# Kernel optimization log

Measured on AMD Instinct MI355X. Metric: run time of the kernel, lower is better.

## Reference

```python
import jax, jax.numpy as jnp
import numpy as np

D = 1536; H = 12; DH = 128; B = 1; S_TXT = 512; S_IMG = 1024; S = S_TXT + S_IMG; FF = 4 * D
EPS = 1e-6


def setup_inputs() -> dict:
    key = jax.random.key(0)
    ks = iter(jax.random.split(key, 64))
    def nrm(shape, s=1.0):
        return jax.random.normal(next(ks), shape, jnp.float32) * s
    w = 0.02
    inp = {}
    inp["hidden_states"] = nrm((B, S_IMG, D))
    inp["encoder_hidden_states"] = nrm((B, S_TXT, D))
    inp["temb"] = nrm((B, D))
    ang = jax.random.uniform(next(ks), (B, S, DH // 2), jnp.float32, 0.0, 2.0 * np.pi)
    c, s = jnp.cos(ang), jnp.sin(ang)
    rot = jnp.stack([jnp.stack([c, -s], -1), jnp.stack([s, c], -1)], -2)  # [B,S,DH/2,2,2]
    inp["image_rotary_emb"] = rot.reshape(1, 1, B * S, DH // 2, 2, 2)
    inp["adaln_img_w"] = nrm((D, 6 * D), w); inp["adaln_img_b"] = jnp.zeros((6 * D,), jnp.float32)
    inp["adaln_txt_w"] = nrm((D, 6 * D), w); inp["adaln_txt_b"] = jnp.zeros((6 * D,), jnp.float32)
    inp["qkv_img_w"] = nrm((D, 3 * D), w); inp["qkv_img_b"] = jnp.zeros((3 * D,), jnp.float32)
    inp["qkv_txt_w"] = nrm((D, 3 * D), w); inp["qkv_txt_b"] = jnp.zeros((3 * D,), jnp.float32)
    inp["q_norm_img"] = jnp.ones((DH,), jnp.float32); inp["k_norm_img"] = jnp.ones((DH,), jnp.float32)
    inp["q_norm_txt"] = jnp.ones((DH,), jnp.float32); inp["k_norm_txt"] = jnp.ones((DH,), jnp.float32)
    inp["out_img_w"] = nrm((D, D), w); inp["out_img_b"] = jnp.zeros((D,), jnp.float32)
    inp["out_txt_w"] = nrm((D, D), w); inp["out_txt_b"] = jnp.zeros((D,), jnp.float32)
    inp["mlp_img_w1"] = nrm((D, FF), w); inp["mlp_img_b1"] = jnp.zeros((FF,), jnp.float32)
    inp["mlp_img_w2"] = nrm((FF, D), w); inp["mlp_img_b2"] = jnp.zeros((D,), jnp.float32)
    inp["mlp_txt_w1"] = nrm((D, FF), w); inp["mlp_txt_b1"] = jnp.zeros((FF,), jnp.float32)
    inp["mlp_txt_w2"] = nrm((FF, D), w); inp["mlp_txt_b2"] = jnp.zeros((D,), jnp.float32)
    return inp


def _ln(x):  # LayerNorm, no affine
    m = jnp.mean(x, -1, keepdims=True)
    v = jnp.mean(jnp.square(x - m), -1, keepdims=True)
    return (x - m) * jax.lax.rsqrt(v + EPS)


def _rms(x, w):  # per-head RMSNorm
    return x * jax.lax.rsqrt(jnp.mean(jnp.square(x), -1, keepdims=True) + EPS) * w


def _rope(x, rot):  # x [B,H,S,DH], rot [B,S,DH/2,2,2]
    xp = x.reshape(*x.shape[:-1], DH // 2, 2)
    out = jnp.einsum('bsdij,bhsdj->bhsdi', rot, xp)
    return out.reshape(x.shape)


def _qkv(x, w, b, qn, kn):  # -> q,k,v each [B,H,S,DH]
    bb, ss, _ = x.shape
    qkv = (x @ w + b).reshape(bb, ss, 3, H, DH).transpose(2, 0, 3, 1, 4)
    q, k, v = qkv[0], qkv[1], qkv[2]
    return _rms(q, qn), _rms(k, kn), v


def _block(hidden_states, encoder_hidden_states, temb, rot,
           adaln_img_w, adaln_img_b, adaln_txt_w, adaln_txt_b,
           qkv_img_w, qkv_img_b, qkv_txt_w, qkv_txt_b,
           q_norm_img, k_norm_img, q_norm_txt, k_norm_txt,
           out_img_w, out_img_b, out_txt_w, out_txt_b,
           mlp_img_w1, mlp_img_b1, mlp_img_w2, mlp_img_b2,
           mlp_txt_w1, mlp_txt_b1, mlp_txt_w2, mlp_txt_b2):
    bsz = hidden_states.shape[0]
    s_txt = encoder_hidden_states.shape[1]
    t = jax.nn.silu(temb)
    emb_i = t @ adaln_img_w + adaln_img_b
    emb_t = t @ adaln_txt_w + adaln_txt_b
    sh_i, sc_i, g_i, shm_i, scm_i, gm_i = [e[:, None, :] for e in jnp.split(emb_i, 6, -1)]
    sh_t, sc_t, g_t, shm_t, scm_t, gm_t = [e[:, None, :] for e in jnp.split(emb_t, 6, -1)]

    n_img = _ln(hidden_states) * (1.0 + sc_i) + sh_i
    n_txt = _ln(encoder_hidden_states) * (1.0 + sc_t) + sh_t

    qi, ki, vi = _qkv(n_img, qkv_img_w, qkv_img_b, q_norm_img, k_norm_img)
    qt, kt, vt = _qkv(n_txt, qkv_txt_w, qkv_txt_b, q_norm_txt, k_norm_txt)
    q = jnp.concatenate([qt, qi], axis=2)
    k = jnp.concatenate([kt, ki], axis=2)
    v = jnp.concatenate([vt, vi], axis=2)

    rot = rot.reshape(bsz, q.shape[2], DH // 2, 2, 2)
    q = _rope(q, rot)
    k = _rope(k, rot)

    scale = 1.0 / np.sqrt(DH)
    attn = jax.nn.softmax(jnp.einsum('bhqd,bhkd->bhqk', q, k) * scale, axis=-1)
    o = jnp.einsum('bhqk,bhkd->bhqd', attn, v)          # [B,H,S,DH]
    o = o.transpose(0, 2, 1, 3).reshape(bsz, -1, D)     # [B,S,D]
    a_txt, a_img = o[:, :s_txt], o[:, s_txt:]

    hidden_states = hidden_states + g_i * (a_img @ out_img_w + out_img_b)
    encoder_hidden_states = encoder_hidden_states + g_t * (a_txt @ out_txt_w + out_txt_b)

    n2_img = _ln(hidden_states) * (1.0 + scm_i) + shm_i
    ff_img = jax.nn.gelu(n2_img @ mlp_img_w1 + mlp_img_b1, approximate=True) @ mlp_img_w2 + mlp_img_b2
    hidden_states = hidden_states + gm_i * ff_img

    n2_txt = _ln(encoder_hidden_states) * (1.0 + scm_t) + shm_t
    ff_txt = jax.nn.gelu(n2_txt @ mlp_txt_w1 + mlp_txt_b1, approximate=True) @ mlp_txt_w2 + mlp_txt_b2
    encoder_hidden_states = encoder_hidden_states + gm_t * ff_txt

    return jnp.concatenate([encoder_hidden_states, hidden_states], axis=1)


def reference(hidden_states, encoder_hidden_states, temb, image_rotary_emb,
              adaln_img_w, adaln_img_b, adaln_txt_w, adaln_txt_b,
              qkv_img_w, qkv_img_b, qkv_txt_w, qkv_txt_b,
              q_norm_img, k_norm_img, q_norm_txt, k_norm_txt,
              out_img_w, out_img_b, out_txt_w, out_txt_b,
              mlp_img_w1, mlp_img_b1, mlp_img_w2, mlp_img_b2,
              mlp_txt_w1, mlp_txt_b1, mlp_txt_w2, mlp_txt_b2):
    s_txt = encoder_hidden_states.shape[1]
    out = _block(hidden_states, encoder_hidden_states, temb, image_rotary_emb,
                 adaln_img_w, adaln_img_b, adaln_txt_w, adaln_txt_b,
                 qkv_img_w, qkv_img_b, qkv_txt_w, qkv_txt_b,
                 q_norm_img, k_norm_img, q_norm_txt, k_norm_txt,
                 out_img_w, out_img_b, out_txt_w, out_txt_b,
                 mlp_img_w1, mlp_img_b1, mlp_img_w2, mlp_img_b2,
                 mlp_txt_w1, mlp_txt_b1, mlp_txt_w2, mlp_txt_b2)
    return (out[:, :s_txt], out[:, s_txt:])
```

## Files before the change

kernel.cpp:

```cpp
#include <hip/hip_runtime.h>
#include <hip/hip_bf16.h>

typedef __bf16 bf16_t;
typedef __attribute__((ext_vector_type(4))) float f32x4;
typedef __attribute__((ext_vector_type(8))) bf16_t bf16x8;
typedef __attribute__((ext_vector_type(4))) bf16_t bf16x4;
typedef __attribute__((ext_vector_type(2))) bf16_t bf16x2;

#define D_MODEL 1536
#define NH 12
#define DHD 128
#define S_TXT 512
#define S_TOT 1536
#define FF_DIM 6144
#define KVSPLIT 4

__device__ inline void gload16(const void* g, void* l) {
    __builtin_amdgcn_global_load_lds((const __attribute__((address_space(1))) unsigned int*)g,
                                     (__attribute__((address_space(3))) unsigned int*)l, 16, 0, 0);
}

__global__ __launch_bounds__(256)
void adaln_p(const float* __restrict__ temb,
             const float* __restrict__ w_img, const float* __restrict__ w_txt,
             float* __restrict__ part) {
    __shared__ float t[192];
    int tid = threadIdx.x;
    int k0 = blockIdx.y * 192;
    if (tid < 192) {
        float x = temb[k0 + tid];
        t[tid] = x / (1.0f + __expf(-x));
    }
    __syncthreads();
    int n_g = blockIdx.x * 256 + tid;
    bool img = n_g < 9216;
    const float* W = img ? w_img : w_txt;
    int n = img ? n_g : n_g - 9216;
    float acc = 0.f;
    for (int kk = 0; kk < 192; kk += 4) {
        acc += t[kk]     * W[(size_t)(k0 + kk) * 9216 + n];
        acc += t[kk + 1] * W[(size_t)(k0 + kk + 1) * 9216 + n];
        acc += t[kk + 2] * W[(size_t)(k0 + kk + 2) * 9216 + n];
        acc += t[kk + 3] * W[(size_t)(k0 + kk + 3) * 9216 + n];
    }
    part[(size_t)blockIdx.y * 18432 + n_g] = acc;
}

__global__ __launch_bounds__(256)
void adaln_r(const float* __restrict__ part,
             const float* __restrict__ b_img, const float* __restrict__ b_txt,
             float* __restrict__ emb_img, float* __restrict__ emb_txt) {
    int n_g = blockIdx.x * 256 + threadIdx.x;
    float a = 0.f;
#pragma unroll
    for (int kc = 0; kc < 8; ++kc) a += part[(size_t)kc * 18432 + n_g];
    if (n_g < 9216) emb_img[n_g] = a + b_img[n_g];
    else            emb_txt[n_g - 9216] = a + b_txt[n_g - 9216];
}

__global__ __launch_bounds__(256)
void ln_mod(const float* __restrict__ src_txt, const float* __restrict__ src_img,
            const float* __restrict__ emb_t, const float* __restrict__ emb_i,
            int sh_c, int sc_c, bf16_t* __restrict__ out) {
    int row = blockIdx.x;
    bool txt = row < S_TXT;
    const float* src = txt ? src_txt + (size_t)row * D_MODEL
                           : src_img + (size_t)(row - S_TXT) * D_MODEL;
    const float* emb = txt ? emb_t : emb_i;
    int tid = threadIdx.x;
    float2 v[3];
    float s = 0.f, sq = 0.f;
#pragma unroll
    for (int i = 0; i < 3; ++i) {
        v[i] = *(const float2*)(src + tid * 2 + 512 * i);
        s  += v[i].x + v[i].y;
        sq += v[i].x * v[i].x + v[i].y * v[i].y;
    }
#pragma unroll
    for (int off = 32; off > 0; off >>= 1) {
        s  += __shfl_down(s, off);
        sq += __shfl_down(sq, off);
    }
    __shared__ float red[8];
    int wave = tid >> 6, lane = tid & 63;
    if (lane == 0) { red[wave] = s; red[4 + wave] = sq; }
    __syncthreads();
    float ts = red[0] + red[1] + red[2] + red[3];
    float tq = red[4] + red[5] + red[6] + red[7];
    float mean = ts * (1.0f / D_MODEL);
    float var  = tq * (1.0f / D_MODEL) - mean * mean;
    float rstd = rsqrtf(var + 1e-6f);
    bf16_t* op = out + (size_t)row * D_MODEL;
#pragma unroll
    for (int i = 0; i < 3; ++i) {
        int c0 = tid * 2 + 512 * i;
        bf16x2 r;
        r[0] = (bf16_t)((v[i].x - mean) * rstd * (1.0f + emb[sc_c * D_MODEL + c0])     + emb[sh_c * D_MODEL + c0]);
        r[1] = (bf16_t)((v[i].y - mean) * rstd * (1.0f + emb[sc_c * D_MODEL + c0 + 1]) + emb[sh_c * D_MODEL + c0 + 1]);
        *(bf16x2*)(op + c0) = r;
    }
}

template <int K, int N>
__global__ __launch_bounds__(256)
void conv_wt(const float* __restrict__ w_t, const float* __restrict__ w_i,
             bf16_t* __restrict__ dst) {
    __shared__ float tile[64][65];
    const float* src = blockIdx.z ? w_i : w_t;
    bf16_t* d = dst + (size_t)blockIdx.z * N * K;
    int bn = blockIdx.x * 64, bk = blockIdx.y * 64;
    int tid = threadIdx.x;
#pragma unroll
    for (int j = 0; j < 4; ++j) {
        int k = (tid >> 4) + 16 * j, c4 = tid & 15;
        float4 v = *(const float4*)(src + (size_t)(bk + k) * N + bn + c4 * 4);
        tile[k][c4 * 4 + 0] = v.x;
        tile[k][c4 * 4 + 1] = v.y;
        tile[k][c4 * 4 + 2] = v.z;
        tile[k][c4 * 4 + 3] = v.w;
    }
    __syncthreads();
#pragma unroll
    for (int j = 0; j < 4; ++j) {
        int n = (tid >> 4) + 16 * j, k4 = tid & 15;
        bf16x4 o;
        o[0] = (bf16_t)tile[k4 * 4 + 0][n];
        o[1] = (bf16_t)tile[k4 * 4 + 1][n];
        o[2] = (bf16_t)tile[k4 * 4 + 2][n];
        o[3] = (bf16_t)tile[k4 * 4 + 3][n];
        *(bf16x4*)(d + (size_t)(bn + n) * K + bk + k4 * 4) = o;
    }
}

template <int EPI>
__global__ __launch_bounds__(512)
void gemmW(const bf16_t* __restrict__ A, int lda,
           const bf16_t* __restrict__ Wt, int ldw, int wimg_off,
           const float* __restrict__ bias_t, const float* __restrict__ bias_i,
           bf16_t* __restrict__ out, bf16_t* __restrict__ out_alt, int ldo, int Ks) {
    __shared__ bf16_t As[128 * 64];
    __shared__ bf16_t Bs[128 * 64];
    const int tid = threadIdx.x;

    const int nbx = gridDim.x;
    const int lb0 = blockIdx.y * nbx + blockIdx.x;
    const int CC = nbx >> 2;
    const int xcd = lb0 & 7, c = lb0 >> 3;
    const int bmT = (xcd & 1) * 6 + (c % 6);
    const int bnT = (xcd >> 1) * CC + (c / 6);
    const int bm = bmT * 128, bn = bnT * 128;
    const int koff = blockIdx.z * Ks;

    const bool txt = bm < S_TXT;
    const bf16_t* W = txt ? Wt : Wt + wimg_off;
    const float* bias = txt ? bias_t : bias_i;
    const int wid = tid >> 6, lane = tid & 63;
    const int wm = wid >> 1, wn = wid & 1;
    const int lr = lane & 15, lg = lane >> 4;

    const int srow = wid * 8 + (lane >> 3);
    const int csrc = ((lane & 7) ^ ((lane >> 3) & 7)) * 8;
    const bf16_t* pA0 = A + (size_t)(bm + srow) * lda + koff + csrc;
    const bf16_t* pA1 = pA0 + (size_t)64 * lda;
    const bf16_t* pB0 = W + (size_t)(bn + srow) * ldw + koff + csrc;
    const bf16_t* pB1 = pB0 + (size_t)64 * ldw;
    const int ldst = (wid * 8) * 64;

    int offA[2][2], offB[4][2];
#pragma unroll
    for (int m = 0; m < 2; ++m)
#pragma unroll
        for (int kk = 0; kk < 2; ++kk)
            offA[m][kk] = (wm * 32 + m * 16 + lr) * 64 + (((kk * 4 + lg) ^ (lr & 7)) * 8);
#pragma unroll
    for (int n = 0; n < 4; ++n)
#pragma unroll
        for (int kk = 0; kk < 2; ++kk)
            offB[n][kk] = (wn * 64 + n * 16 + lr) * 64 + (((kk * 4 + lg) ^ (lr & 7)) * 8);

    f32x4 acc[2][4] = {};
    const int nt = Ks >> 6;

    for (int t = 0; t < nt; ++t) {
        gload16(pA0, &As[ldst]);
        gload16(pA1, &As[ldst + 64 * 64]);
        gload16(pB0, &Bs[ldst]);
        gload16(pB1, &Bs[ldst + 64 * 64]);
        pA0 += 64; pA1 += 64; pB0 += 64; pB1 += 64;
        __syncthreads();
#pragma unroll
        for (int kk = 0; kk < 2; ++kk) {
            bf16x8 af[2], bfm[4];
#pragma unroll
            for (int m = 0; m < 2; ++m) af[m] = *(const bf16x8*)&As[offA[m][kk]];
#pragma unroll
            for (int n = 0; n < 4; ++n) bfm[n] = *(const bf16x8*)&Bs[offB[n][kk]];
#pragma unroll
            for (int m = 0; m < 2; ++m)
#pragma unroll
                for (int n = 0; n < 4; ++n)
                    acc[m][n] = __builtin_amdgcn_mfma_f32_16x16x32_bf16(af[m], bfm[n], acc[m][n], 0, 0, 0);
        }
        __syncthreads();
    }

    bf16_t* obase = out;
    if constexpr (EPI == 3)
        obase = (blockIdx.z < 2) ? out + (size_t)blockIdx.z * S_TOT * ldo
                                 : out_alt + (size_t)(blockIdx.z - 2) * S_TOT * ldo;
#pragma unroll
    for (int m = 0; m < 2; ++m) {
#pragma unroll
        for (int r = 0; r < 4; ++r) {
            int grow = bm + wm * 32 + m * 16 + lg * 4 + r;
#pragma unroll
            for (int n = 0; n < 4; ++n) {
                int gcol = bn + wn * 64 + n * 16 + lr;
                float v = acc[m][n][r];
                if constexpr (EPI == 0) {
                    v += bias[gcol];
                } else if constexpr (EPI == 1) {
                    float x = v + bias[gcol];
                    float th = tanhf(0.7978845608028654f * (x + 0.044715f * x * x * x));
                    v = 0.5f * x * (1.0f + th);
                }
                obase[(size_t)grow * ldo + gcol] = (bf16_t)v;
            }
        }
    }
}

template <int NS>
__global__ __launch_bounds__(256)
void gemm_red(const bf16_t* __restrict__ p, const bf16_t* __restrict__ p_alt,
              const float* __restrict__ bias_t, const float* __restrict__ bias_i,
              const float* __restrict__ gate_t, const float* __restrict__ gate_i,
              const float* __restrict__ resid_t, const float* __restrict__ resid_i,
              float* __restrict__ out) {
    int r = blockIdx.x;
    bool txt = r < S_TXT;
    const float* bias = txt ? bias_t : bias_i;
    const float* gate = txt ? gate_t : gate_i;
    const float* resid = txt ? resid_t + (size_t)r * D_MODEL
                             : resid_i + (size_t)(r - S_TXT) * D_MODEL;
    int tid = threadIdx.x;
#pragma unroll
    for (int i = 0; i < 3; ++i) {
        int c = tid * 2 + 512 * i;
        float v0 = 0.f, v1 = 0.f;
#pragma unroll
        for (int s = 0; s < NS; ++s) {
            const bf16_t* ps = (s < 2) ? p + (size_t)s * S_TOT * D_MODEL
                                       : p_alt + (size_t)(s - 2) * S_TOT * D_MODEL;
            bf16x2 t2 = *(const bf16x2*)&ps[(size_t)r * D_MODEL + c];
            v0 += (float)t2[0];
            v1 += (float)t2[1];
        }
        float2 o;
        o.x = resid[c]     + gate[c]     * (v0 + bias[c]);
        o.y = resid[c + 1] + gate[c + 1] * (v1 + bias[c + 1]);
        *(float2*)&out[(size_t)r * D_MODEL + c] = o;
    }
}

__global__ __launch_bounds__(256)
void red_ln(const bf16_t* __restrict__ p,
            const float* __restrict__ bias_t, const float* __restrict__ bias_i,
            const float* __restrict__ gate_t, const float* __restrict__ gate_i,
            const float* __restrict__ resid_t, const float* __restrict__ resid_i,
            const float* __restrict__ emb_t, const float* __restrict__ emb_i,
            float* __restrict__ out, bf16_t* __restrict__ nout) {
    int r = blockIdx.x;
    bool txt = r < S_TXT;
    const float* bias = txt ? bias_t : bias_i;
    const float* gate = txt ? gate_t : gate_i;
    const float* resid = txt ? resid_t + (size_t)r * D_MODEL
                             : resid_i + (size_t)(r - S_TXT) * D_MODEL;
    const float* emb = txt ? emb_t : emb_i;
    int tid = threadIdx.x;
    float2 v[3];
    float s = 0.f, sq = 0.f;
#pragma unroll
    for (int i = 0; i < 3; ++i) {
        int c = tid * 2 + 512 * i;
        bf16x2 p0 = *(const bf16x2*)&p[(size_t)r * D_MODEL + c];
        bf16x2 p1 = *(const bf16x2*)&p[(size_t)(S_TOT + r) * D_MODEL + c];
        float2 o;
        o.x = resid[c]     + gate[c]     * ((float)p0[0] + (float)p1[0] + bias[c]);
        o.y = resid[c + 1] + gate[c + 1] * ((float)p0[1] + (float)p1[1] + bias[c + 1]);
        *(float2*)&out[(size_t)r * D_MODEL + c] = o;
        v[i] = o;
        s  += o.x + o.y;
        sq += o.x * o.x + o.y * o.y;
    }
#pragma unroll
    for (int off = 32; off > 0; off >>= 1) {
        s  += __shfl_down(s, off);
        sq += __shfl_down(sq, off);
    }
    __shared__ float red[8];
    int wave = tid >> 6, lane = tid & 63;
    if (lane == 0) { red[wave] = s; red[4 + wave] = sq; }
    __syncthreads();
    float ts = red[0] + red[1] + red[2] + red[3];
    float tq = red[4] + red[5] + red[6] + red[7];
    float mean = ts * (1.0f / D_MODEL);
    float var  = tq * (1.0f / D_MODEL) - mean * mean;
    float rstd = rsqrtf(var + 1e-6f);
    bf16_t* op = nout + (size_t)r * D_MODEL;
#pragma unroll
    for (int i = 0; i < 3; ++i) {
        int c0 = tid * 2 + 512 * i;
        bf16x2 o2;
        o2[0] = (bf16_t)((v[i].x - mean) * rstd * (1.0f + emb[4 * D_MODEL + c0])     + emb[3 * D_MODEL + c0]);
        o2[1] = (bf16_t)((v[i].y - mean) * rstd * (1.0f + emb[4 * D_MODEL + c0 + 1]) + emb[3 * D_MODEL + c0 + 1]);
        *(bf16x2*)(op + c0) = o2;
    }
}

__global__ __launch_bounds__(256)
void qkv_post(const bf16_t* __restrict__ qkv, const float* __restrict__ rope,
              const float* __restrict__ qn_i, const float* __restrict__ kn_i,
              const float* __restrict__ qn_t, const float* __restrict__ kn_t,
              bf16_t* __restrict__ qb, bf16_t* __restrict__ kb,
              bf16_t* __restrict__ vt) {
    int h = blockIdx.x, sb = blockIdx.y * 64;
    int tid = threadIdx.x, wave = tid >> 6, lane = tid & 63;

#pragma unroll 4
    for (int it = 0; it < 16; ++it) {
        int s = sb + it * 4 + wave;
        bool txt = s < S_TXT;
        const float* qn = txt ? qn_t : qn_i;
        const float* kn = txt ? kn_t : kn_i;
        const bf16_t* base = qkv + (size_t)s * 4608 + h * DHD + lane * 2;
        bf16x2 qv = *(const bf16x2*)base;
        bf16x2 kv = *(const bf16x2*)(base + D_MODEL);
        float q0 = (float)qv[0], q1 = (float)qv[1];
        float k0 = (float)kv[0], k1 = (float)kv[1];
        float qs = q0 * q0 + q1 * q1, ks = k0 * k0 + k1 * k1;
#pragma unroll
        for (int mask = 32; mask > 0; mask >>= 1) {
            qs += __shfl_xor(qs, mask);
            ks += __shfl_xor(ks, mask);
        }
        float qr = rsqrtf(qs * (1.0f / DHD) + 1e-6f);
        float kr = rsqrtf(ks * (1.0f / DHD) + 1e-6f);
        float2 qn2 = *(const float2*)(qn + lane * 2);
        float2 kn2 = *(const float2*)(kn + lane * 2);
        q0 *= qr * qn2.x; q1 *= qr * qn2.y;
        k0 *= kr * kn2.x; k1 *= kr * kn2.y;
        float4 rp = *(const float4*)(rope + ((size_t)s * 64 + lane) * 4);
        float oq0 = rp.x * q0 + rp.y * q1, oq1 = rp.z * q0 + rp.w * q1;
        float ok0 = rp.x * k0 + rp.y * k1, ok1 = rp.z * k0 + rp.w * k1;
        size_t idx = ((size_t)h * S_TOT + s) * DHD + lane * 2;
        bf16x2 qo, ko;
        qo[0] = (bf16_t)(oq0 * 0.08838834764831845f);
        qo[1] = (bf16_t)(oq1 * 0.08838834764831845f);
        ko[0] = (bf16_t)ok0; ko[1] = (bf16_t)ok1;
        *(bf16x2*)&qb[idx] = qo;
        *(bf16x2*)&kb[idx] = ko;
    }

    __shared__ bf16_t tile[64][130];
#pragma unroll
    for (int j = 0; j < 32; ++j) {
        int linear = tid + 256 * j;
        int sl = linear >> 7, dh = linear & 127;
        tile[sl][dh] = qkv[(size_t)(sb + sl) * 4608 + 2 * D_MODEL + h * DHD + dh];
    }
    __syncthreads();
#pragma unroll
    for (int j = 0; j < 32; ++j) {
        int linear = tid + 256 * j;
        int dh = linear >> 6, sl = linear & 63;
        vt[((size_t)h * DHD + dh) * S_TOT + sb + sl] = tile[sl][dh];
    }
}

__global__ __launch_bounds__(512)
void attn_k(const bf16_t* __restrict__ qbuf, const bf16_t* __restrict__ kbuf,
            const bf16_t* __restrict__ vt,
            float* __restrict__ part_o, float* __restrict__ part_ml) {
    __shared__ bf16_t Ks[64 * 128];
    __shared__ bf16_t Vs[128 * 64];
    __shared__ bf16_t P[8][16 * 64];
    int h = blockIdx.x, qblk = blockIdx.y, z = blockIdx.z;
    int q0 = qblk * 128;
    int tid = threadIdx.x, wid = tid >> 6, lane = tid & 63;
    int lr = lane & 15, lg = lane >> 4;

    const bf16_t* Qp = qbuf + ((size_t)h * S_TOT + q0 + wid * 16 + lr) * DHD;
    bf16x8 qf[4];
#pragma unroll
    for (int kk = 0; kk < 4; ++kk) qf[kk] = *(const bf16x8*)(Qp + (kk * 4 + lg) * 8);

    const int sKr = wid * 4 + (lane >> 4);
    const int cK = lane & 15;
    const bf16_t* Kb = kbuf + ((size_t)h * S_TOT + sKr) * DHD + ((cK ^ (sKr & 7)) * 8);
    const int sVr = wid * 8 + (lane >> 3);
    const int cV = lane & 7;
    const bf16_t* Vb = vt + ((size_t)h * DHD + sVr) * S_TOT + ((cV ^ (sVr & 7)) * 8);

    f32x4 of[8] = {};
    float m[4] = {-1e30f, -1e30f, -1e30f, -1e30f};
    float l[4] = {};
    const int kv0 = z * (S_TOT / KVSPLIT);
    const int nt = (S_TOT / KVSPLIT) / 64;

    for (int t = 0; t < nt; ++t) {
        const int kb0 = kv0 + t * 64;
#pragma unroll
        for (int j = 0; j < 2; ++j) {
            gload16(Kb + (size_t)(kb0 + j * 32) * DHD, &Ks[(wid * 4) * 128 + j * 4096]);
            gload16(Vb + kb0 + (size_t)j * 64 * S_TOT, &Vs[(wid * 8) * 64 + j * 4096]);
        }
        asm volatile("s_waitcnt vmcnt(0)" ::: "memory");
        __builtin_amdgcn_s_barrier();
        f32x4 sf[4] = {};
        __builtin_amdgcn_s_setprio(1);
#pragma unroll
        for (int n = 0; n < 4; ++n) {
#pragma unroll
            for (int kk = 0; kk < 4; ++kk) {
                bf16x8 kf = *(const bf16x8*)&Ks[(n * 16 + lr) * 128 + (((kk * 4 + lg) ^ (lr & 7)) * 8)];
                sf[n] = __builtin_amdgcn_mfma_f32_16x16x32_bf16(qf[kk], kf, sf[n], 0, 0, 0);
            }
        }
        __builtin_amdgcn_s_setprio(0);
        float bm[4], alpha[4], rs[4];
#pragma unroll
        for (int r = 0; r < 4; ++r)
            bm[r] = fmaxf(fmaxf(sf[0][r], sf[1][r]), fmaxf(sf[2][r], sf[3][r]));
#pragma unroll
        for (int mask = 1; mask < 16; mask <<= 1)
#pragma unroll
            for (int r = 0; r < 4; ++r) bm[r] = fmaxf(bm[r], __shfl_xor(bm[r], mask));
#pragma unroll
        for (int r = 0; r < 4; ++r) {
            float mn = fmaxf(m[r], bm[r]);
            alpha[r] = __expf(m[r] - mn);
            m[r] = mn;
            rs[r] = 0.f;
        }
#pragma unroll
        for (int n = 0; n < 4; ++n)
#pragma unroll
            for (int r = 0; r < 4; ++r) {
                float p = __expf(sf[n][r] - m[r]);
                rs[r] += p;
                int row = lg * 4 + r, col = n * 16 + lr;
                P[wid][row * 64 + ((((col >> 3) ^ (row & 7)) << 3) | (col & 7))] = (bf16_t)p;
            }
#pragma unroll
        for (int mask = 1; mask < 16; mask <<= 1)
#pragma unroll
            for (int r = 0; r < 4; ++r) rs[r] += __shfl_xor(rs[r], mask);
#pragma unroll
        for (int r = 0; r < 4; ++r) l[r] = l[r] * alpha[r] + rs[r];
#pragma unroll
        for (int nf = 0; nf < 8; ++nf)
#pragma unroll
            for (int r = 0; r < 4; ++r) of[nf][r] *= alpha[r];
        __builtin_amdgcn_s_setprio(1);
#pragma unroll
        for (int kk2 = 0; kk2 < 2; ++kk2) {
            bf16x8 pf = *(const bf16x8*)&P[wid][lr * 64 + (((kk2 * 4 + lg) ^ (lr & 7)) * 8)];
#pragma unroll
            for (int nf = 0; nf < 8; ++nf) {
                bf16x8 vf = *(const bf16x8*)&Vs[(nf * 16 + lr) * 64 + (((kk2 * 4 + lg) ^ (lr & 7)) * 8)];
                of[nf] = __builtin_amdgcn_mfma_f32_16x16x32_bf16(pf, vf, of[nf], 0, 0, 0);
            }
        }
        __builtin_amdgcn_s_setprio(0);
        __builtin_amdgcn_s_barrier();
    }
    int hq = h * 12 + qblk;
    float* po = part_o + ((size_t)z * 144 + hq) * 16384;
    int rb = wid * 16 + lg * 4;
#pragma unroll
    for (int r = 0; r < 4; ++r)
#pragma unroll
        for (int nf = 0; nf < 8; ++nf)
            po[(rb + r) * 128 + nf * 16 + lr] = of[nf][r];
    if (lr == 0) {
#pragma unroll
        for (int r = 0; r < 4; ++r) {
            size_t mi = (((size_t)z * 144 + hq) * 128 + rb + r) * 2;
            part_ml[mi]     = m[r];
            part_ml[mi + 1] = l[r];
        }
    }
}

__global__ __launch_bounds__(256)
void attn_red(const float* __restrict__ part_o, const float* __restrict__ part_ml,
              bf16_t* __restrict__ o) {
    int b = blockIdx.x;
    int h = b / 24, qi = b % 24;
    int hq = h * 12 + (qi >> 1), roff = (qi & 1) * 64;
    int q0 = qi * 64;
    __shared__ float wz[KVSPLIT][64];
    __shared__ float invL[64];
    int tid = threadIdx.x;
    if (tid < 64) {
        float mz[KVSPLIT], lz[KVSPLIT];
#pragma unroll
        for (int zz = 0; zz < KVSPLIT; ++zz) {
            size_t mi = (((size_t)zz * 144 + hq) * 128 + roff + tid) * 2;
            mz[zz] = part_ml[mi];
            lz[zz] = part_ml[mi + 1];
        }
        float M = mz[0];
#pragma unroll
        for (int zz = 1; zz < KVSPLIT; ++zz) M = fmaxf(M, mz[zz]);
        float L = 0.f;
#pragma unroll
        for (int zz = 0; zz < KVSPLIT; ++zz) {
            float w = __expf(mz[zz] - M);
            wz[zz][tid] = w;
            L += w * lz[zz];
        }
        invL[tid] = 1.0f / L;
    }
    __syncthreads();
#pragma unroll
    for (int i = 0; i < 8; ++i) {
        int e4 = tid + 256 * i;
        int row = e4 >> 5, c4 = e4 & 31;
        f32x4 acc = {};
#pragma unroll
        for (int zz = 0; zz < KVSPLIT; ++zz) {
            f32x4 v = *(const f32x4*)&part_o[((size_t)zz * 144 + hq) * 16384 + (roff + row) * 128 + c4 * 4];
            float w = wz[zz][row];
            acc[0] += v[0] * w; acc[1] += v[1] * w; acc[2] += v[2] * w; acc[3] += v[3] * w;
        }
        float il = invL[row];
        bf16x4 r;
        r[0] = (bf16_t)(acc[0] * il); r[1] = (bf16_t)(acc[1] * il);
        r[2] = (bf16_t)(acc[2] * il); r[3] = (bf16_t)(acc[3] * il);
        *(bf16x4*)&o[(size_t)(q0 + row) * D_MODEL + h * DHD + c4 * 4] = r;
    }
}

extern "C" void kernel_launch(void* const* d_in, const int* in_sizes, int n_in,
                              void* d_out, int out_size, void* d_ws, size_t ws_size,
                              hipStream_t stream) {
    const float* hidden  = (const float*)d_in[0];
    const float* encoder = (const float*)d_in[1];
    const float* temb    = (const float*)d_in[2];
    const float* rope    = (const float*)d_in[3];
    const float* adaln_img_w = (const float*)d_in[4];
    const float* adaln_img_b = (const float*)d_in[5];
    const float* adaln_txt_w = (const float*)d_in[6];
    const float* adaln_txt_b = (const float*)d_in[7];
    const float* qkv_img_w = (const float*)d_in[8];
    const float* qkv_img_b = (const float*)d_in[9];
    const float* qkv_txt_w = (const float*)d_in[10];
    const float* qkv_txt_b = (const float*)d_in[11];
    const float* qn_img = (const float*)d_in[12];
    const float* kn_img = (const float*)d_in[13];
    const float* qn_txt = (const float*)d_in[14];
    const float* kn_txt = (const float*)d_in[15];
    const float* out_img_w = (const float*)d_in[16];
    const float* out_img_b = (const float*)d_in[17];
    const float* out_txt_w = (const float*)d_in[18];
    const float* out_txt_b = (const float*)d_in[19];
    const float* mlp_img_w1 = (const float*)d_in[20];
    const float* mlp_img_b1 = (const float*)d_in[21];
    const float* mlp_img_w2 = (const float*)d_in[22];
    const float* mlp_img_b2 = (const float*)d_in[23];
    const float* mlp_txt_w1 = (const float*)d_in[24];
    const float* mlp_txt_b1 = (const float*)d_in[25];
    const float* mlp_txt_w2 = (const float*)d_in[26];
    const float* mlp_txt_b2 = (const float*)d_in[27];
    float* dout = (float*)d_out;
    char* wsb = (char*)d_ws;

    float*  emb_i = (float*)(wsb);
    float*  emb_t = (float*)(wsb + 36864);
    bf16_t* wreg  = (bf16_t*)(wsb + 73728);
    float*  part  = (float*)(wsb + 73728);
    float*  part_o = (float*)(wsb + 73728);
    bf16_t* n1    = (bf16_t*)(wsb + 37822464);
    float*  part_ml = (float*)(wsb + 37822464);
    bf16_t* qkvb  = (bf16_t*)(wsb + 42541056);
    bf16_t* obuf  = qkvb;
    bf16_t* ffb   = qkvb + 2359296;
    bf16_t* qb    = (bf16_t*)(wsb + 56696832);
    bf16_t* kb    = (bf16_t*)(wsb + 61415424);
    bf16_t* vt    = (bf16_t*)(wsb + 66134016);
    bf16_t* pout = (bf16_t*)(wsb + 47259648);
    bf16_t* pm2  = (bf16_t*)(wsb + 37822464);
    bf16_t* pm2b = (bf16_t*)(wsb + 66134016);

    adaln_p<<<dim3(72, 8), 256, 0, stream>>>(temb, adaln_img_w, adaln_txt_w, part);
    adaln_r<<<72, 256, 0, stream>>>(part, adaln_img_b, adaln_txt_b, emb_i, emb_t);
    ln_mod<<<S_TOT, 256, 0, stream>>>(encoder, hidden, emb_t, emb_i, 0, 1, n1);
    conv_wt<1536, 4608><<<dim3(72, 24, 2), 256, 0, stream>>>(qkv_txt_w, qkv_img_w, wreg);
    gemmW<0><<<dim3(36, 12), 512, 0, stream>>>(
        n1, D_MODEL, wreg, 1536, 4608 * 1536, qkv_txt_b, qkv_img_b,
        qkvb, nullptr, 4608, 1536);
    qkv_post<<<dim3(12, 24), 256, 0, stream>>>(qkvb, rope, qn_img, kn_img, qn_txt, kn_txt,
                                               qb, kb, vt);
    attn_k<<<dim3(12, 12, KVSPLIT), 512, 0, stream>>>(qb, kb, vt, part_o, part_ml);
    attn_red<<<288, 256, 0, stream>>>(part_o, part_ml, obuf);
    conv_wt<1536, 1536><<<dim3(24, 24, 2), 256, 0, stream>>>(out_txt_w, out_img_w, wreg);
    gemmW<3><<<dim3(12, 12, 2), 512, 0, stream>>>(
        obuf, D_MODEL, wreg, 1536, 1536 * 1536, nullptr, nullptr,
        pout, nullptr, D_MODEL, 768);
    red_ln<<<S_TOT, 256, 0, stream>>>(
        pout, out_txt_b, out_img_b,
        emb_t + 2 * D_MODEL, emb_i + 2 * D_MODEL, encoder, hidden,
        emb_t, emb_i, dout, n1);
    conv_wt<1536, 6144><<<dim3(96, 24, 2), 256, 0, stream>>>(mlp_txt_w1, mlp_img_w1, wreg);
    gemmW<1><<<dim3(48, 12), 512, 0, stream>>>(
        n1, D_MODEL, wreg, 1536, 6144 * 1536, mlp_txt_b1, mlp_img_b1,
        ffb, nullptr, FF_DIM, 1536);
    conv_wt<6144, 1536><<<dim3(24, 96, 2), 256, 0, stream>>>(mlp_txt_w2, mlp_img_w2, wreg);
    gemmW<3><<<dim3(12, 12, 3), 512, 0, stream>>>(
        ffb, FF_DIM, wreg, 6144, 1536 * 6144, nullptr, nullptr,
        pm2, pm2b, D_MODEL, 2048);
    gemm_red<3><<<S_TOT, 256, 0, stream>>>(
        pm2, pm2b, mlp_txt_b2, mlp_img_b2,
        emb_t + 5 * D_MODEL, emb_i + 5 * D_MODEL,
        dout, dout + (size_t)S_TXT * D_MODEL, dout);
    (void)in_sizes; (void)n_in; (void)out_size; (void)ws_size;
}
```

Baseline: 318.7 us.

## Double-buffer LDS tiles in gemmW to overlap global loads with MFMA

```diff
diff --git a/kernel.cpp b/kernel.cpp
--- a/kernel.cpp
+++ b/kernel.cpp
@@ -138,8 +138,8 @@
            const bf16_t* __restrict__ Wt, int ldw, int wimg_off,
            const float* __restrict__ bias_t, const float* __restrict__ bias_i,
            bf16_t* __restrict__ out, bf16_t* __restrict__ out_alt, int ldo, int Ks) {
-    __shared__ bf16_t As[128 * 64];
-    __shared__ bf16_t Bs[128 * 64];
+    __shared__ bf16_t As[2][128 * 64];
+    __shared__ bf16_t Bs[2][128 * 64];
     const int tid = threadIdx.x;
 
     const int nbx = gridDim.x;
@@ -181,27 +181,39 @@
     f32x4 acc[2][4] = {};
     const int nt = Ks >> 6;
 
+    gload16(pA0, &As[0][ldst]);
+    gload16(pA1, &As[0][ldst + 64 * 64]);
+    gload16(pB0, &Bs[0][ldst]);
+    gload16(pB1, &Bs[0][ldst + 64 * 64]);
+    pA0 += 64; pA1 += 64; pB0 += 64; pB1 += 64;
+
     for (int t = 0; t < nt; ++t) {
-        gload16(pA0, &As[ldst]);
-        gload16(pA1, &As[ldst + 64 * 64]);
-        gload16(pB0, &Bs[ldst]);
-        gload16(pB1, &Bs[ldst + 64 * 64]);
-        pA0 += 64; pA1 += 64; pB0 += 64; pB1 += 64;
-        __syncthreads();
+        const int cur = t & 1, nxt = cur ^ 1;
+        if (t + 1 < nt) {
+            gload16(pA0, &As[nxt][ldst]);
+            gload16(pA1, &As[nxt][ldst + 64 * 64]);
+            gload16(pB0, &Bs[nxt][ldst]);
+            gload16(pB1, &Bs[nxt][ldst + 64 * 64]);
+            pA0 += 64; pA1 += 64; pB0 += 64; pB1 += 64;
+            asm volatile("s_waitcnt vmcnt(4)" ::: "memory");
+        } else {
+            asm volatile("s_waitcnt vmcnt(0)" ::: "memory");
+        }
+        __builtin_amdgcn_s_barrier();
 #pragma unroll
         for (int kk = 0; kk < 2; ++kk) {
             bf16x8 af[2], bfm[4];
 #pragma unroll
-            for (int m = 0; m < 2; ++m) af[m] = *(const bf16x8*)&As[offA[m][kk]];
-#pragma unroll
-            for (int n = 0; n < 4; ++n) bfm[n] = *(const bf16x8*)&Bs[offB[n][kk]];
+            for (int m = 0; m < 2; ++m) af[m] = *(const bf16x8*)&As[cur][offA[m][kk]];
+#pragma unroll
+            for (int n = 0; n < 4; ++n) bfm[n] = *(const bf16x8*)&Bs[cur][offB[n][kk]];
 #pragma unroll
             for (int m = 0; m < 2; ++m)
 #pragma unroll
                 for (int n = 0; n < 4; ++n)
                     acc[m][n] = __builtin_amdgcn_mfma_f32_16x16x32_bf16(af[m], bfm[n], acc[m][n], 0, 0, 0);
         }
-        __syncthreads();
+        __builtin_amdgcn_s_barrier();
     }
 
     bf16_t* obase = out;
```

Measured after the change: 329.2 us. +3.3%, slower.
